# Kernel tuning notes

Hardware: AMD Instinct MI355X
Metric: run time of the kernel (lower is better)

The kernel has to match this reference:

```python
import jax, jax.numpy as jnp
import numpy as np

B, N, D, H = 4, 1024, 512, 8
HID = 4 * H  # bias_mlp hidden width


def setup_inputs() -> dict:
    key = jax.random.key(0)
    ks = jax.random.split(key, 8)
    x = jax.random.normal(ks[0], (B, N, D), jnp.float32)
    coords = jax.random.uniform(ks[1], (B, N, 3), jnp.float32)
    mask = jnp.zeros((B, N), dtype=bool)  # src_key_padding_mask (no padding)
    qkv_w = jax.random.normal(ks[2], (D, 3 * D), jnp.float32) * (1.0 / np.sqrt(D))
    out_w = jax.random.normal(ks[3], (D, D), jnp.float32) * (1.0 / np.sqrt(D))
    out_b = jnp.zeros((D,), jnp.float32)
    w1 = jax.random.normal(ks[4], (3, HID), jnp.float32) * (1.0 / np.sqrt(3.0))
    b1 = jnp.zeros((HID,), jnp.float32)
    w2 = jax.random.normal(ks[5], (HID, H), jnp.float32) * (1.0 / np.sqrt(HID))
    b2 = jnp.zeros((H,), jnp.float32)
    return dict(x=x, coords=coords, mask=mask, qkv_w=qkv_w, out_w=out_w,
                out_b=out_b, w1=w1, b1=b1, w2=w2, b2=b2)


def reference(x, coords, mask, qkv_w, out_w, out_b, w1, b1, w2, b2):
    b, n, d = x.shape
    h = w2.shape[1]
    dh = d // h
    scale = dh ** (-0.5)
    qkv = x @ qkv_w
    q, k, v = jnp.split(qkv, 3, axis=-1)
    q = q.reshape(b, n, h, dh).transpose(0, 2, 1, 3)
    k = k.reshape(b, n, h, dh).transpose(0, 2, 1, 3)
    v = v.reshape(b, n, h, dh).transpose(0, 2, 1, 3)
    # Pairwise relative positions: [B,N,N,3]
    dpos = coords[:, :, None, :] - coords[:, None, :, :]
    # bias MLP: Linear -> exact GELU -> Linear, then permute to [B,H,N,N]
    hidden = jax.nn.gelu(dpos @ w1 + b1, approximate=False)
    bias = (hidden @ w2 + b2).transpose(0, 3, 1, 2)
    dots = jnp.einsum('bhid,bhjd->bhij', q, k) * scale
    logits = dots + bias
    logits = jnp.where(mask[:, None, None, :], -jnp.inf, logits)
    attn = jax.nn.softmax(logits, axis=-1)
    out = jnp.einsum('bhij,bhjd->bhid', attn, v)
    out = out.transpose(0, 2, 1, 3).reshape(b, n, d)
    return out @ out_w + out_b
```

## Files before the change

### kernel.cpp

```cpp
#include <hip/hip_runtime.h>
#include <hip/hip_bf16.h>
#include <hip/hip_fp16.h>
#include <math.h>

#define Bb 4
#define Nn 1024
#define Dd 512
#define Hh 8
#define KP 1536

typedef short bf16x8 __attribute__((ext_vector_type(8)));
typedef _Float16 f16x8 __attribute__((ext_vector_type(8)));
typedef float f32x4  __attribute__((ext_vector_type(4)));

struct __align__(16) H8 { __half2 x, y, z, w; };

static __device__ inline short f2bf(float f) {
    __hip_bfloat16 h = __float2bfloat16(f);
    return __builtin_bit_cast(short, h);
}
static __device__ inline float bf2f(short s) {
    return __builtin_bit_cast(float, ((unsigned int)(unsigned short)s) << 16);
}
static __device__ inline float h2f(short s) {
    return __half2float(__builtin_bit_cast(__half, s));
}

#define GLDS(gp, lp) \
    __builtin_amdgcn_global_load_lds( \
        (const __attribute__((address_space(1))) void*)(gp), \
        (__attribute__((address_space(3))) void*)(lp), 16, 0, 0)

static __device__ inline __half2 gelu2(__half2 x) {
    const __half2 c1  = __half2half2(__float2half(0.1029436f));
    const __half2 c0  = __half2half2(__float2half(2.3022082f));
    const __half2 one = __half2half2(__float2half(1.0f));
    __half2 s = __hmul2(x, x);
    __half2 p = __hfma2(s, c1, c0);
    __half2 e = h2exp2(__hneg2(__hmul2(x, p)));
    __half2 r = h2rcp(__hadd2(e, one));
    return __hmul2(x, r);
}

static __device__ __forceinline__ void convBt_tile(
    const float* __restrict__ W, short* __restrict__ Bt, int N,
    int n0, int k0, float* Wt )
{
    const int t = threadIdx.x;
#pragma unroll
    for (int it = 0; it < 4; it++) {
        int cidx = t + (it << 8);
        int krow = cidx >> 4, nc4 = (cidx & 15) << 2;
        const float4 v = *(const float4*)&W[(size_t)(k0 + krow) * N + n0 + nc4];
        Wt[(nc4 + 0) * 65 + krow] = v.x;
        Wt[(nc4 + 1) * 65 + krow] = v.y;
        Wt[(nc4 + 2) * 65 + krow] = v.z;
        Wt[(nc4 + 3) * 65 + krow] = v.w;
    }
    __syncthreads();
#pragma unroll
    for (int it = 0; it < 4; it++) {
        int cidx = t + (it << 8);
        int nrow = cidx >> 4, kc4 = (cidx & 15) << 2;
        float a = Wt[nrow * 65 + kc4 + 0], b = Wt[nrow * 65 + kc4 + 1];
        float c = Wt[nrow * 65 + kc4 + 2], d = Wt[nrow * 65 + kc4 + 3];
        short4 hi = { f2bf(a), f2bf(b), f2bf(c), f2bf(d) };
        short4 lo = { f2bf(a - bf2f(hi.x)), f2bf(b - bf2f(hi.y)),
                      f2bf(c - bf2f(hi.z)), f2bf(d - bf2f(hi.w)) };
        short* row = Bt + (size_t)(n0 + nrow) * KP + k0 + kc4;
        *(short4*)(row)        = hi;
        *(short4*)(row + 512)  = hi;
        *(short4*)(row + 1024) = lo;
    }
}

__global__ __launch_bounds__(256) void prologue(
    const float* __restrict__ X, const float* __restrict__ qkv_w,
    const float* __restrict__ out_w, const float* __restrict__ coords,
    const float* __restrict__ w1, const float* __restrict__ b1,
    short* __restrict__ Ax, short* __restrict__ Btq, short* __restrict__ Btw,
    float* __restrict__ A_, float* __restrict__ G_)
{
    __shared__ float Wt[64 * 65];
    const int id = blockIdx.x;
    const int t = threadIdx.x;

    if (id < 2048) {
        const size_t i4 = ((size_t)id * 256 + t) * 4;
        const int m = (int)(i4 >> 9), k = (int)(i4 & 511);
        const float4 v = *(const float4*)&X[i4];
        short4 hi = { f2bf(v.x), f2bf(v.y), f2bf(v.z), f2bf(v.w) };
        short4 lo = { f2bf(v.x - bf2f(hi.x)), f2bf(v.y - bf2f(hi.y)),
                      f2bf(v.z - bf2f(hi.z)), f2bf(v.w - bf2f(hi.w)) };
        short* row = Ax + (size_t)m * KP + k;
        *(short4*)(row)        = hi;
        *(short4*)(row + 512)  = lo;
        *(short4*)(row + 1024) = hi;
    } else if (id < 2048 + 192) {
        const int rr = id - 2048;
        convBt_tile(qkv_w, Btq, 1536, (rr % 24) << 6, (rr / 24) << 6, Wt);
    } else if (id < 2048 + 192 + 64) {
        const int rr = id - 2240;
        convBt_tile(out_w, Btw, 512, (rr & 7) << 6, (rr >> 3) << 6, Wt);
    } else {
        float* sw1 = Wt;
        float* sb1 = Wt + 96;
        if (t < 96) sw1[t] = w1[t];
        if (t < 32) sb1[t] = b1[t];
        __syncthreads();
        const int idx = (id - 2304) * 256 + t;
        const int b  = idx >> 13;
        const int i  = (idx >> 3) & 1023;
        const int k4 = (idx & 7) << 2;
        const float cx = coords[((size_t)(b * Nn + i)) * 3 + 0];
        const float cy = coords[((size_t)(b * Nn + i)) * 3 + 1];
        const float cz = coords[((size_t)(b * Nn + i)) * 3 + 2];
        float4 av, gv;
        float* avp = (float*)&av; float* gvp = (float*)&gv;
#pragma unroll
        for (int e = 0; e < 4; e++) {
            int k = k4 + e;
            float g = fmaf(cx, sw1[k], fmaf(cy, sw1[32 + k], cz * sw1[64 + k]));
            gvp[e] = g;
            avp[e] = g + sb1[k];
        }
        *(float4*)&A_[((size_t)(b * Nn + i)) * 32 + k4] = av;
        *(float4*)&G_[((size_t)(b * Nn + i)) * 32 + k4] = gv;
    }
}

__global__ __launch_bounds__(256) void gemm_qkv(
    const short* __restrict__ A, const short* __restrict__ Bt,
    short* __restrict__ Cbf, int N)
{
    __shared__ __align__(16) short As[2 * 128 * 32];
    __shared__ __align__(16) short Bs[2 * 64 * 32];

    const int t    = threadIdx.x;
    const int lane = t & 63;
    const int w    = t >> 6;
    const int r    = lane & 15;
    const int q    = lane >> 4;
    const int wy   = w >> 1, wx = w & 1;
    const int bm = blockIdx.y << 7, bn = blockIdx.x << 6;

    const int grow = 32 * w + (lane >> 2);
    const int gcol = (lane & 3) << 3;
    const short* Ag = A + (size_t)(bm + grow) * KP + gcol;
    const int wB = w & 1, hB = w >> 1;
    const short* Bg = Bt + (size_t)(bn + 32 * wB + (lane >> 2)) * KP + gcol + 32 * hB;
    short* AsW  = As + w * 1024;
    short* AsW2 = As + 4096 + w * 1024;
    short* BsW  = Bs + hB * 2048 + wB * 1024;

    f32x4 acc[4][2] = {};

    for (int k0 = 0; k0 < KP; k0 += 64) {
        __syncthreads();
        GLDS(Ag + k0,                AsW);
        GLDS(Ag + 16 * KP + k0,      AsW + 512);
        GLDS(Ag + k0 + 32,           AsW2);
        GLDS(Ag + 16 * KP + k0 + 32, AsW2 + 512);
        GLDS(Bg + k0,                BsW);
        GLDS(Bg + 16 * KP + k0,      BsW + 512);
        __syncthreads();

#pragma unroll
        for (int hh = 0; hh < 2; hh++) {
            bf16x8 af[4], bfr[2];
#pragma unroll
            for (int i = 0; i < 4; i++)
                af[i] = *(const bf16x8*)&As[hh * 4096 + (64 * wy + 16 * i + r) * 32 + q * 8];
#pragma unroll
            for (int j = 0; j < 2; j++)
                bfr[j] = *(const bf16x8*)&Bs[hh * 2048 + (32 * wx + 16 * j + r) * 32 + q * 8];
#pragma unroll
            for (int i = 0; i < 4; i++)
#pragma unroll
                for (int j = 0; j < 2; j++)
                    acc[i][j] = __builtin_amdgcn_mfma_f32_16x16x32_bf16(af[i], bfr[j], acc[i][j], 0, 0, 0);
        }
    }

#pragma unroll
    for (int i = 0; i < 4; i++) {
#pragma unroll
        for (int j = 0; j < 2; j++) {
            const int col = bn + 32 * wx + 16 * j + r;
#pragma unroll
            for (int g = 0; g < 4; g++) {
                const int row = bm + 64 * wy + 16 * i + 4 * q + g;
                Cbf[(size_t)row * N + col] = f2bf(acc[i][j][g]);
            }
        }
    }
}

__global__ __launch_bounds__(256) void gemm_out(
    const short* __restrict__ A, const short* __restrict__ Bt,
    float* __restrict__ Cf, const float* __restrict__ bias, int N)
{
    __shared__ __align__(16) short As[2 * 64 * 32];
    __shared__ __align__(16) short Bs[2 * 64 * 32];

    const int t    = threadIdx.x;
    const int lane = t & 63;
    const int w    = t >> 6;
    const int r    = lane & 15;
    const int q    = lane >> 4;
    const int wy   = w >> 1, wx = w & 1;
    const int bm = blockIdx.y << 6, bn = blockIdx.x << 6;

    const int grow = 16 * w + (lane >> 2);
    const int gcol = (lane & 3) << 3;
    const short* Ag = A  + (size_t)(bm + grow) * KP + gcol;
    const short* Bg = Bt + (size_t)(bn + grow) * KP + gcol;
    short* AsW  = As + w * 512;
    short* AsW2 = As + 2048 + w * 512;
    short* BsW  = Bs + w * 512;
    short* BsW2 = Bs + 2048 + w * 512;

    f32x4 acc[2][2] = {};

    for (int k0 = 0; k0 < KP; k0 += 64) {
        __syncthreads();
        GLDS(Ag + k0,      AsW);
        GLDS(Ag + k0 + 32, AsW2);
        GLDS(Bg + k0,      BsW);
        GLDS(Bg + k0 + 32, BsW2);
        __syncthreads();

#pragma unroll
        for (int hh = 0; hh < 2; hh++) {
            bf16x8 af[2], bfr[2];
#pragma unroll
            for (int i = 0; i < 2; i++)
                af[i] = *(const bf16x8*)&As[hh * 2048 + (32 * wy + 16 * i + r) * 32 + q * 8];
#pragma unroll
            for (int j = 0; j < 2; j++)
                bfr[j] = *(const bf16x8*)&Bs[hh * 2048 + (32 * wx + 16 * j + r) * 32 + q * 8];
#pragma unroll
            for (int i = 0; i < 2; i++)
#pragma unroll
                for (int j = 0; j < 2; j++)
                    acc[i][j] = __builtin_amdgcn_mfma_f32_16x16x32_bf16(af[i], bfr[j], acc[i][j], 0, 0, 0);
        }
    }

#pragma unroll
    for (int i = 0; i < 2; i++) {
#pragma unroll
        for (int j = 0; j < 2; j++) {
            const int col = bn + 32 * wx + 16 * j + r;
#pragma unroll
            for (int g = 0; g < 4; g++) {
                const int row = bm + 32 * wy + 16 * i + 4 * q + g;
                Cf[(size_t)row * N + col] = acc[i][j][g] + bias[col];
            }
        }
    }
}

__global__ __launch_bounds__(256) void bias_mlp3(
    const float* __restrict__ A_, const float* __restrict__ G_,
    const float* __restrict__ w2, const float* __restrict__ b2,
    __half* __restrict__ biasc)
{
    __shared__ float Wls[4 * 8 * 72];

    const int t    = threadIdx.x;
    const int lane = t & 63;
    const int w    = t >> 6;
    const int r    = lane & 15;
    const int q    = lane >> 4;

    const int b   = blockIdx.z;
    const int i0  = blockIdx.y << 3;
    const int j0w = (blockIdx.x << 8) + (w << 6);

    f16x8 bw2;
#pragma unroll
    for (int e = 0; e < 8; e++)
        bw2[e] = (r < 8) ? (_Float16)w2[(q * 8 + e) * 8 + r] : (_Float16)0.0f;

    float4 gv0[4], gv1[4];
#pragma unroll
    for (int t4 = 0; t4 < 4; t4++) {
        const int j = j0w + 16 * t4 + r;
        gv0[t4] = *(const float4*)&G_[((size_t)(b * Nn + j)) * 32 + q * 8];
        gv1[t4] = *(const float4*)&G_[((size_t)(b * Nn + j)) * 32 + q * 8 + 4];
    }

    const int h   = lane >> 3;
    const int j8  = (lane & 7) << 3;
    const float b2h = b2[h];
    const int jt  = j0w >> 6;
    const int nt  = (j8 >> 4) & 3;
    const int rc0 = j8 & 15;

#pragma unroll 2
    for (int ii = 0; ii < 8; ii++) {
        const int i = i0 + ii;
        const float4 av0 = *(const float4*)&A_[((size_t)(b * Nn + i)) * 32 + q * 8];
        const float4 av1 = *(const float4*)&A_[((size_t)(b * Nn + i)) * 32 + q * 8 + 4];

#pragma unroll
        for (int t4 = 0; t4 < 4; t4++) {
            __half2 x0 = __floats2half2_rn(av0.x - gv0[t4].x, av0.y - gv0[t4].y);
            __half2 x1 = __floats2half2_rn(av0.z - gv0[t4].z, av0.w - gv0[t4].w);
            __half2 x2 = __floats2half2_rn(av1.x - gv1[t4].x, av1.y - gv1[t4].y);
            __half2 x3 = __floats2half2_rn(av1.z - gv1[t4].z, av1.w - gv1[t4].w);
            __half2 h0 = gelu2(x0), h1 = gelu2(x1);
            __half2 h2 = gelu2(x2), h3 = gelu2(x3);
            f16x8 afr;
            ((__half2*)&afr)[0] = h0;
            ((__half2*)&afr)[1] = h1;
            ((__half2*)&afr)[2] = h2;
            ((__half2*)&afr)[3] = h3;
            f32x4 d = {};
            d = __builtin_amdgcn_mfma_f32_16x16x32_f16(afr, bw2, d, 0, 0, 0);
            if (r < 8) {
#pragma unroll
                for (int g = 0; g < 4; g++)
                    Wls[(w * 8 + r) * 72 + 16 * t4 + 4 * q + g] = d[g];
            }
        }

        float4 o0 = *(const float4*)&Wls[(w * 8 + h) * 72 + j8];
        float4 o1 = *(const float4*)&Wls[(w * 8 + h) * 72 + j8 + 4];
        H8 hv;
        hv.x = __floats2half2_rn(o0.x + b2h, o0.y + b2h);
        hv.y = __floats2half2_rn(o0.z + b2h, o0.w + b2h);
        hv.z = __floats2half2_rn(o1.x + b2h, o1.y + b2h);
        hv.w = __floats2half2_rn(o1.z + b2h, o1.w + b2h);

        const int bi = i >> 6, wr = (i >> 4) & 3, qc = (i >> 2) & 3, gc = i & 3;
        size_t off = ((((((size_t)(b * Hh + h) * 16 + bi) * 16 + jt) * 4 + wr) * 16
                       + (nt * 4 + gc)) << 6) + qc * 16 + rc0;
        *(H8*)&biasc[off] = hv;
    }
}

__global__ __launch_bounds__(512, 4) void attn_full(
    const short* __restrict__ qkv, const __half* __restrict__ biasc,
    short* __restrict__ Ao)
{
    __shared__ __align__(16) short Kls[64 * 72];
    __shared__ __align__(16) short Vt [64 * 72];
    __shared__ __align__(16) short Pls[64 * 72];
    __shared__ float lred[8][16];

    const int t    = threadIdx.x;
    const int lane = t & 63;
    const int w    = t >> 6;
    const int sw   = w & 3;
    const int ch   = w >> 2;
    const int r    = lane & 15;
    const int q    = lane >> 4;

    const int id    = blockIdx.x;
    const int itile = id & 15;
    const int h     = (id >> 4) & 7;
    const int b     = id >> 7;
    const int i0g   = itile << 6;

    const short* qbase = qkv + ((size_t)(b * Nn + i0g + 16 * sw + r)) * KP + h * 64;
    const bf16x8 aq0 = *(const bf16x8*)(qbase + q * 8);
    const bf16x8 aq1 = *(const bf16x8*)(qbase + 32 + q * 8);

    const int srow = t >> 3;
    const int sc8  = (t & 7) << 3;

    bf16x8 kf, vf;
    {
        const short* base = qkv + ((size_t)(b * Nn + srow)) * KP + h * 64 + sc8;
        kf = *(const bf16x8*)(base + 512);
        vf = *(const bf16x8*)(base + 1024);
    }

    f32x4 accO[2] = {};
    float lsum[4] = { 0.f, 0.f, 0.f, 0.f };

    const __half* bpb = biasc
        + (((((size_t)(b * Hh + h) * 16 + itile) * 16) * 4 + sw) << 10)
        + lane;

    for (int jt = 0; jt < 16; jt++) {
        *(bf16x8*)&Kls[srow * 72 + sc8] = kf;
#pragma unroll
        for (int e = 0; e < 8; e++) {
            int d = sc8 + e;
            Vt[d * 72 + (srow ^ ((d & 28) << 1))] = vf[e];
        }
        __syncthreads();

        const __half* bpj = bpb + ((size_t)jt << 12);
        float bv[8];
#pragma unroll
        for (int u = 0; u < 8; u++)
            bv[u] = __half2float(bpj[(8 * ch + u) << 6]);

        if (jt < 15) {
            const short* base = qkv + ((size_t)(b * Nn + ((jt + 1) << 6) + srow)) * KP + h * 64 + sc8;
            kf = *(const bf16x8*)(base + 512);
            vf = *(const bf16x8*)(base + 1024);
        }

        f32x4 accS[2] = {};
#pragma unroll
        for (int nt = 0; nt < 2; nt++) {
            const bf16x8 bk0 = *(const bf16x8*)&Kls[(32 * ch + 16 * nt + r) * 72 + q * 8];
            const bf16x8 bk1 = *(const bf16x8*)&Kls[(32 * ch + 16 * nt + r) * 72 + 32 + q * 8];
            accS[nt] = __builtin_amdgcn_mfma_f32_16x16x32_bf16(aq0, bk0, accS[nt], 0, 0, 0);
            accS[nt] = __builtin_amdgcn_mfma_f32_16x16x32_bf16(aq1, bk1, accS[nt], 0, 0, 0);
        }

#pragma unroll
        for (int nt = 0; nt < 2; nt++) {
#pragma unroll
            for (int g = 0; g < 4; g++) {
                float p = __expf(fmaf(accS[nt][g], 0.125f, bv[nt * 4 + g]));
                lsum[g] += p;
                Pls[(16 * sw + 4 * q + g) * 72 + 32 * ch + 16 * nt + r] = f2bf(p);
            }
        }
        __syncthreads();

        const bf16x8 ap0 = *(const bf16x8*)&Pls[(16 * sw + r) * 72 + q * 8];
        const bf16x8 ap1 = *(const bf16x8*)&Pls[(16 * sw + r) * 72 + 32 + q * 8];
#pragma unroll
        for (int nt = 0; nt < 2; nt++) {
            const int n = 32 * ch + 16 * nt + r;
            const int swr = (n & 28) << 1;
            const bf16x8 bv0 = *(const bf16x8*)&Vt[n * 72 + ((8 * q) ^ swr)];
            const bf16x8 bv1 = *(const bf16x8*)&Vt[n * 72 + ((32 + 8 * q) ^ swr)];
            accO[nt] = __builtin_amdgcn_mfma_f32_16x16x32_bf16(ap0, bv0, accO[nt], 0, 0, 0);
            accO[nt] = __builtin_amdgcn_mfma_f32_16x16x32_bf16(ap1, bv1, accO[nt], 0, 0, 0);
        }
        __syncthreads();
    }

#pragma unroll
    for (int g = 0; g < 4; g++)
#pragma unroll
        for (int off = 1; off < 16; off <<= 1)
            lsum[g] += __shfl_xor(lsum[g], off);

    if (r == 0) {
#pragma unroll
        for (int g = 0; g < 4; g++)
            lred[w][4 * q + g] = lsum[g];
    }
    __syncthreads();

    float linv[4];
#pragma unroll
    for (int g = 0; g < 4; g++)
        linv[g] = 1.0f / (lred[sw][4 * q + g] + lred[sw + 4][4 * q + g]);

    const size_t rowb = (size_t)(b * Nn + i0g + 16 * sw + 4 * q);
#pragma unroll
    for (int nt = 0; nt < 2; nt++) {
        const int col = h * 64 + 32 * ch + 16 * nt + r;
#pragma unroll
        for (int g = 0; g < 4; g++) {
            float v = accO[nt][g] * linv[g];
            short hi = f2bf(v);
            short lo = f2bf(v - bf2f(hi));
            short* rp = Ao + (rowb + g) * KP + col;
            rp[0]    = hi;
            rp[512]  = lo;
            rp[1024] = hi;
        }
    }
}

extern "C" void kernel_launch(void* const* d_in, const int* in_sizes, int n_in,
                              void* d_out, int out_size, void* d_ws, size_t ws_size,
                              hipStream_t stream)
{
    (void)in_sizes; (void)n_in; (void)out_size; (void)ws_size;
    const float* x      = (const float*)d_in[0];
    const float* coords = (const float*)d_in[1];
    const float* qkv_w  = (const float*)d_in[3];
    const float* out_w  = (const float*)d_in[4];
    const float* out_b  = (const float*)d_in[5];
    const float* w1     = (const float*)d_in[6];
    const float* b1     = (const float*)d_in[7];
    const float* w2     = (const float*)d_in[8];
    const float* b2     = (const float*)d_in[9];
    float* out = (float*)d_out;

    char* p = (char*)d_ws;
    short* qkvb = (short*)p;  p += (size_t)4096 * KP * 2;
    short* Ax   = (short*)p;  p += (size_t)4096 * KP * 2;
    short* Btq  = (short*)p;  p += (size_t)1536 * KP * 2;
    short* Ao   = (short*)p;  p += (size_t)4096 * KP * 2;
    short* Btw  = (short*)p;  p += (size_t)512  * KP * 2;
    float* A_   = (float*)p;  p += (size_t)Bb * Nn * 32 * 4;
    float* G_   = (float*)p;  p += (size_t)Bb * Nn * 32 * 4;
    __half* biasc = (__half*)p; p += (size_t)Bb * Hh * Nn * Nn * 2;

    dim3 blk(256);
    prologue<<<2432, blk, 0, stream>>>(x, qkv_w, out_w, coords, w1, b1,
                                       Ax, Btq, Btw, A_, G_);
    gemm_qkv<<<dim3(1536 / 64, 4096 / 128), blk, 0, stream>>>(Ax, Btq, qkvb, 1536);
    bias_mlp3<<<dim3(4, 128, 4), blk, 0, stream>>>(A_, G_, w2, b2, biasc);
    attn_full<<<512, dim3(512), 0, stream>>>(qkvb, biasc, Ao);
    gemm_out<<<dim3(512 / 64, 4096 / 64), blk, 0, stream>>>(Ao, Btw, out, out_b, 512);
}
```

Before: 204.4 us.

## Double-buffer K/V shared tiles in attention kernel to drop a barrier per iteration

K and V shared-memory tiles are now double-buffered. The next tile is written into the alternate buffer before the barrier that already follows the P write, which removes one __syncthreads per loop iteration. Bias loads move after the prefetch global loads. In exchange, shared memory use grows by about 18KB per block, which may lower occupancy at 4 blocks of 512 threads per CU.

```diff
diff --git a/kernel.cpp b/kernel.cpp
--- a/kernel.cpp
+++ b/kernel.cpp
@@ -345,8 +345,8 @@
     const short* __restrict__ qkv, const __half* __restrict__ biasc,
     short* __restrict__ Ao)
 {
-    __shared__ __align__(16) short Kls[64 * 72];
-    __shared__ __align__(16) short Vt [64 * 72];
+    __shared__ __align__(16) short Kls[2][64 * 72];
+    __shared__ __align__(16) short Vt [2][64 * 72];
     __shared__ __align__(16) short Pls[64 * 72];
     __shared__ float lred[8][16];
 
@@ -371,12 +371,18 @@
     const int srow = t >> 3;
     const int sc8  = (t & 7) << 3;
 
-    bf16x8 kf, vf;
     {
         const short* base = qkv + ((size_t)(b * Nn + srow)) * KP + h * 64 + sc8;
-        kf = *(const bf16x8*)(base + 512);
-        vf = *(const bf16x8*)(base + 1024);
-    }
+        bf16x8 k0 = *(const bf16x8*)(base + 512);
+        bf16x8 v0 = *(const bf16x8*)(base + 1024);
+        *(bf16x8*)&Kls[0][srow * 72 + sc8] = k0;
+#pragma unroll
+        for (int e = 0; e < 8; e++) {
+            int d = sc8 + e;
+            Vt[0][d * 72 + (srow ^ ((d & 28) << 1))] = v0[e];
+        }
+    }
+    __syncthreads();
 
     f32x4 accO[2] = {};
     float lsum[4] = { 0.f, 0.f, 0.f, 0.f };
@@ -385,32 +391,26 @@
         + (((((size_t)(b * Hh + h) * 16 + itile) * 16) * 4 + sw) << 10)
         + lane;
 
+    int cur = 0;
     for (int jt = 0; jt < 16; jt++) {
-        *(bf16x8*)&Kls[srow * 72 + sc8] = kf;
-#pragma unroll
-        for (int e = 0; e < 8; e++) {
-            int d = sc8 + e;
-            Vt[d * 72 + (srow ^ ((d & 28) << 1))] = vf[e];
-        }
-        __syncthreads();
-
-        const __half* bpj = bpb + ((size_t)jt << 12);
-        float bv[8];
-#pragma unroll
-        for (int u = 0; u < 8; u++)
-            bv[u] = __half2float(bpj[(8 * ch + u) << 6]);
-
+        bf16x8 kf, vf;
         if (jt < 15) {
             const short* base = qkv + ((size_t)(b * Nn + ((jt + 1) << 6) + srow)) * KP + h * 64 + sc8;
             kf = *(const bf16x8*)(base + 512);
             vf = *(const bf16x8*)(base + 1024);
         }
 
+        const __half* bpj = bpb + ((size_t)jt << 12);
+        float bv[8];
+#pragma unroll
+        for (int u = 0; u < 8; u++)
+            bv[u] = __half2float(bpj[(8 * ch + u) << 6]);
+
         f32x4 accS[2] = {};
 #pragma unroll
         for (int nt = 0; nt < 2; nt++) {
-            const bf16x8 bk0 = *(const bf16x8*)&Kls[(32 * ch + 16 * nt + r) * 72 + q * 8];
-            const bf16x8 bk1 = *(const bf16x8*)&Kls[(32 * ch + 16 * nt + r) * 72 + 32 + q * 8];
+            const bf16x8 bk0 = *(const bf16x8*)&Kls[cur][(32 * ch + 16 * nt + r) * 72 + q * 8];
+            const bf16x8 bk1 = *(const bf16x8*)&Kls[cur][(32 * ch + 16 * nt + r) * 72 + 32 + q * 8];
             accS[nt] = __builtin_amdgcn_mfma_f32_16x16x32_bf16(aq0, bk0, accS[nt], 0, 0, 0);
             accS[nt] = __builtin_amdgcn_mfma_f32_16x16x32_bf16(aq1, bk1, accS[nt], 0, 0, 0);
         }
@@ -424,6 +424,15 @@
                 Pls[(16 * sw + 4 * q + g) * 72 + 32 * ch + 16 * nt + r] = f2bf(p);
             }
         }
+
+        if (jt < 15) {
+            *(bf16x8*)&Kls[cur ^ 1][srow * 72 + sc8] = kf;
+#pragma unroll
+            for (int e = 0; e < 8; e++) {
+                int d = sc8 + e;
+                Vt[cur ^ 1][d * 72 + (srow ^ ((d & 28) << 1))] = vf[e];
+            }
+        }
         __syncthreads();
 
         const bf16x8 ap0 = *(const bf16x8*)&Pls[(16 * sw + r) * 72 + q * 8];
@@ -432,12 +441,13 @@
         for (int nt = 0; nt < 2; nt++) {
             const int n = 32 * ch + 16 * nt + r;
             const int swr = (n & 28) << 1;
-            const bf16x8 bv0 = *(const bf16x8*)&Vt[n * 72 + ((8 * q) ^ swr)];
-            const bf16x8 bv1 = *(const bf16x8*)&Vt[n * 72 + ((32 + 8 * q) ^ swr)];
+            const bf16x8 bv0 = *(const bf16x8*)&Vt[cur][n * 72 + ((8 * q) ^ swr)];
+            const bf16x8 bv1 = *(const bf16x8*)&Vt[cur][n * 72 + ((32 + 8 * q) ^ swr)];
             accO[nt] = __builtin_amdgcn_mfma_f32_16x16x32_bf16(ap0, bv0, accO[nt], 0, 0, 0);
             accO[nt] = __builtin_amdgcn_mfma_f32_16x16x32_bf16(ap1, bv1, accO[nt], 0, 0, 0);
         }
         __syncthreads();
+        cur ^= 1;
     }
 
 #pragma unroll
```

Result: no change. 202.8 us (-0.8%).
